# Kernel tuning notes

Hardware: AMD Instinct MI355X
Metric: run time of the kernel (lower is better)

The kernel has to match this reference:

```python
import jax, jax.numpy as jnp
import numpy as np

B, NBLK, D, DY, NDIM, NMC, DH = 4096, 12, 2, 2, 24, 256, 100
SQRT3 = 3.0 ** 0.5
G2 = np.array([[1.0, 0.0], [0.5, SQRT3 / 2.0]], dtype=np.float32)
G = jnp.asarray(np.kron(np.eye(NBLK, dtype=np.float32), G2))  # (24,24) block-diag hexagonal generator
LOG_VOL = (NDIM // 2) * float(np.log(SQRT3 / 2.0))  # log sqrt(det(G G^T))


def _lin(x, w, b=None):
    y = x @ w.T
    return y if b is None else y + b


def _hex_quantize(y):
    # Exact nearest-point quantizer for the product-of-A2 (hexagonal) lattice.
    p = y.reshape(y.shape[:-1] + (NDIM // 2, 2))
    off = jnp.array([0.5, SQRT3 / 2.0], dtype=y.dtype)
    def rnd(q):  # round to rectangular sublattice Z x sqrt(3)Z
        return jnp.stack([jnp.round(q[..., 0]), jnp.round(q[..., 1] / SQRT3) * SQRT3], axis=-1)
    c0 = rnd(p)
    c1 = rnd(p - off) + off
    d0 = jnp.sum((p - c0) ** 2, axis=-1)
    d1 = jnp.sum((p - c1) ** 2, axis=-1)
    return jnp.where((d0 <= d1)[..., None], c0, c1).reshape(y.shape)


def _logits_cumulative(v, Hs, bs, fs):
    # compressai-style per-channel monotone cumulative network. v: (..., C) -> (..., C)
    v = v[..., None]  # (..., C, 1)
    for k in range(len(Hs)):
        v = jnp.einsum('coi,...ci->...co', jax.nn.softplus(Hs[k]), v) + bs[k][:, :, 0]
        if k < len(fs):
            v = v + jnp.tanh(fs[k][:, :, 0]) * jnp.tanh(v)
    return v[..., 0]


def setup_inputs() -> dict:
    key = jax.random.key(0)
    ks = iter(jax.random.split(key, 64))
    def nrm(shape, s=1.0):
        return jax.random.normal(next(ks), shape, jnp.float32) * s
    inp = {}
    inp['x'] = nrm((B, NBLK, D))
    inp['y_mean'] = nrm((NBLK, DY))
    inp['u'] = jax.random.uniform(next(ks), (NMC, NDIM), jnp.float32)
    inp['ga_w0'] = nrm((DH, D), D ** -0.5); inp['ga_b0'] = jnp.zeros((DH,), jnp.float32)
    inp['ga_w1'] = nrm((DH, DH), DH ** -0.5); inp['ga_b1'] = jnp.zeros((DH,), jnp.float32)
    inp['ga_w2'] = nrm((DY, DH), DH ** -0.5); inp['ga_b2'] = jnp.zeros((DY,), jnp.float32)
    inp['gs_w0'] = nrm((DH, DY), DY ** -0.5); inp['gs_b0'] = jnp.zeros((DH,), jnp.float32)
    inp['gs_w1'] = nrm((DH, DH), DH ** -0.5); inp['gs_b1'] = jnp.zeros((DH,), jnp.float32)
    inp['gs_w2'] = nrm((D, DH), DH ** -0.5); inp['gs_b2'] = jnp.zeros((D,), jnp.float32)
    inp['gac_w0'] = nrm((DH, NDIM), NDIM ** -0.5)
    inp['gac_w1'] = nrm((DH, DH), DH ** -0.5)
    inp['gac_w2'] = nrm((NDIM, DH), DH ** -0.5)
    inp['gsc_w0'] = nrm((DH, NDIM), NDIM ** -0.5)
    inp['gsc_w1'] = nrm((DH, DH), DH ** -0.5)
    inp['gsc_w2'] = nrm((NDIM, DH), DH ** -0.5)
    # factorized-prior cumulative params, layer dims 1->3->3->3->3->1
    inp['eb_H0'] = nrm((NDIM, 3, 1), 0.5)
    inp['eb_H1'] = nrm((NDIM, 3, 3), 0.5)
    inp['eb_H2'] = nrm((NDIM, 3, 3), 0.5)
    inp['eb_H3'] = nrm((NDIM, 3, 3), 0.5)
    inp['eb_H4'] = nrm((NDIM, 1, 3), 0.5)
    inp['eb_b0'] = nrm((NDIM, 3, 1), 0.5)
    inp['eb_b1'] = nrm((NDIM, 3, 1), 0.5)
    inp['eb_b2'] = nrm((NDIM, 3, 1), 0.5)
    inp['eb_b3'] = nrm((NDIM, 3, 1), 0.5)
    inp['eb_b4'] = nrm((NDIM, 1, 1), 0.5)
    inp['eb_a0'] = nrm((NDIM, 3, 1), 0.5)
    inp['eb_a1'] = nrm((NDIM, 3, 1), 0.5)
    inp['eb_a2'] = nrm((NDIM, 3, 1), 0.5)
    inp['eb_a3'] = nrm((NDIM, 3, 1), 0.5)
    return inp


def reference(x, y_mean, u, ga_w0, ga_b0, ga_w1, ga_b1, ga_w2, ga_b2,
              gs_w0, gs_b0, gs_w1, gs_b1, gs_w2, gs_b2,
              gac_w0, gac_w1, gac_w2, gsc_w0, gsc_w1, gsc_w2,
              eb_H0, eb_H1, eb_H2, eb_H3, eb_H4,
              eb_b0, eb_b1, eb_b2, eb_b3, eb_b4,
              eb_a0, eb_a1, eb_a2, eb_a3):
    lrelu, sp = jax.nn.leaky_relu, jax.nn.softplus
    # analysis transform g_a: (B, 12, 2) -> (B, 12, dy)
    y1 = _lin(lrelu(_lin(lrelu(_lin(x, ga_w0, ga_b0)), ga_w1, ga_b1)), ga_w2, ga_b2)
    # EMA zero-mean update (buffer assignment => no gradient through the mean)
    ym = jax.lax.stop_gradient(0.05 * y_mean + 0.95 * jnp.mean(y1, axis=0))
    y1 = (y1 - ym).reshape(B, NDIM)
    # coupled analysis transform g_a_c (Softplus MLP, no bias)
    y1 = _lin(sp(_lin(sp(_lin(y1, gac_w0)), gac_w1)), gac_w2)
    # quasi-uniform samples from the Voronoi cell of the lattice origin
    u2 = u @ G
    u2 = u2 - _hex_quantize(u2)
    # lattice quantization with straight-through estimator
    y_q = _hex_quantize(y1)
    y_hat = y1 + jax.lax.stop_gradient(y_q - y1)
    # Monte-Carlo log-likelihood over the Voronoi cell with factorized prior density
    Hs = (eb_H0, eb_H1, eb_H2, eb_H3, eb_H4)
    bs = (eb_b0, eb_b1, eb_b2, eb_b3, eb_b4)
    fs = (eb_a0, eb_a1, eb_a2, eb_a3)
    pts = y_hat[:, None, :] + u2[None, :, :]  # (B, NMC, NDIM)
    def cdf(p):
        return jax.nn.sigmoid(_logits_cumulative(p, Hs, bs, fs))
    _, pdf = jax.jvp(cdf, (pts,), (jnp.ones_like(pts),))  # density = d/dx cdf(x)
    logp = jnp.sum(jnp.log(pdf + 1e-9), axis=-1)  # (B, NMC)
    lik = jax.scipy.special.logsumexp(logp, axis=1) - jnp.log(jnp.float32(NMC)) + LOG_VOL  # (B,)
    # synthesis transforms
    y_hat1 = _lin(sp(_lin(sp(_lin(y_hat, gsc_w0)), gsc_w1)), gsc_w2).reshape(B, NBLK, DY) + ym
    x_hat = _lin(lrelu(_lin(lrelu(_lin(y_hat1, gs_w0, gs_b0)), gs_w1, gs_b1)), gs_w2, gs_b2)
    return (x_hat, lik)
```

## Files before the change

kernel.cpp:

```cpp
#include <hip/hip_runtime.h>
#include <hip/hip_bf16.h>
#include <math.h>

constexpr int NB    = 4096;
constexpr int NBLKc = 12;
constexpr int NDIMc = 24;
constexpr int NMCc  = 256;
constexpr int ROWS2 = NB * NBLKc;

constexpr size_t WS_Y1    = 0;
constexpr size_t WS_YHAT  = 98304;
constexpr size_t WS_YHAT1 = 196608;
constexpr size_t WS_YM    = 294912;
constexpr size_t WS_U2T   = 294936;
constexpr size_t WS_EB    = 301080;
constexpr size_t WS_KMM   = 302472;
constexpr size_t WS_TBL   = 302520;
constexpr size_t WS_END   = WS_TBL + 24 * 64 * 256;

constexpr float STEP_ODD = 0.8660254037844386f;
constexpr float INV_ODD  = 1.1547005383792517f;

__device__ __forceinline__ float lrelu(float x) { return x >= 0.f ? x : 0.01f * x; }

__device__ __forceinline__ float rcp_fast(float x) { return __builtin_amdgcn_rcpf(x); }

__device__ __forceinline__ float tanh_fast(float x) {
    float xx = fminf(fmaxf(x, -15.f), 15.f);
    float e = __expf(xx + xx);
    return fmaf(-2.f, rcp_fast(e + 1.f), 1.f);
}

__device__ __forceinline__ float splus(float x) {
    return fmaxf(x, 0.f) + __logf(1.f + __expf(-fabsf(x)));
}
__device__ __forceinline__ float splus_precise(float x) {
    return fmaxf(x, 0.f) + log1pf(expf(-fabsf(x)));
}

__device__ __forceinline__ void hexq(float p0, float p1, float& q0, float& q1) {
    const float S3 = 1.7320508075688772f;
    const float H3 = 0.8660254037844386f;
    float c00 = rintf(p0);
    float c01 = rintf(p1 / S3) * S3;
    float c10 = rintf(p0 - 0.5f) + 0.5f;
    float c11 = rintf((p1 - H3) / S3) * S3 + H3;
    float d0 = (p0 - c00) * (p0 - c00) + (p1 - c01) * (p1 - c01);
    float d1 = (p0 - c10) * (p0 - c10) + (p1 - c11) * (p1 - c11);
    bool take0 = d0 <= d1;
    q0 = take0 ? c00 : c10;
    q1 = take0 ? c01 : c11;
}

__device__ __forceinline__ float logpdf_ch(const float* __restrict__ P, float p) {
    float w00 = P[0], w01 = P[1], w02 = P[2];
    float z0 = fmaf(w00, p, P[3]);
    float z1 = fmaf(w01, p, P[4]);
    float z2 = fmaf(w02, p, P[5]);
    float a0 = P[6], a1 = P[7], a2 = P[8];
    float e0 = tanh_fast(z0), e1 = tanh_fast(z1), e2 = tanh_fast(z2);
    float h0 = fmaf(a0, e0, z0), h1 = fmaf(a1, e1, z1), h2 = fmaf(a2, e2, z2);
    float t0 = w00 * fmaf(a0, fmaf(-e0, e0, 1.f), 1.f);
    float t1 = w01 * fmaf(a1, fmaf(-e1, e1, 1.f), 1.f);
    float t2 = w02 * fmaf(a2, fmaf(-e2, e2, 1.f), 1.f);

#define EB_LAYER(O)                                                            \
    {                                                                          \
        float z0n = fmaf(P[O+0], h0, fmaf(P[O+1], h1, fmaf(P[O+2], h2, P[O+9])));  \
        float z1n = fmaf(P[O+3], h0, fmaf(P[O+4], h1, fmaf(P[O+5], h2, P[O+10]))); \
        float z2n = fmaf(P[O+6], h0, fmaf(P[O+7], h1, fmaf(P[O+8], h2, P[O+11]))); \
        float s0 = fmaf(P[O+0], t0, fmaf(P[O+1], t1, P[O+2] * t2));            \
        float s1 = fmaf(P[O+3], t0, fmaf(P[O+4], t1, P[O+5] * t2));            \
        float s2 = fmaf(P[O+6], t0, fmaf(P[O+7], t1, P[O+8] * t2));            \
        float g0 = P[O+12], g1 = P[O+13], g2 = P[O+14];                        \
        float q0 = tanh_fast(z0n), q1 = tanh_fast(z1n), q2 = tanh_fast(z2n);   \
        h0 = fmaf(g0, q0, z0n); h1 = fmaf(g1, q1, z1n); h2 = fmaf(g2, q2, z2n); \
        t0 = s0 * fmaf(g0, fmaf(-q0, q0, 1.f), 1.f);                           \
        t1 = s1 * fmaf(g1, fmaf(-q1, q1, 1.f), 1.f);                           \
        t2 = s2 * fmaf(g2, fmaf(-q2, q2, 1.f), 1.f);                           \
    }
    EB_LAYER(9)
    EB_LAYER(24)
    EB_LAYER(39)
#undef EB_LAYER

    float L = fmaf(P[54], h0, fmaf(P[55], h1, fmaf(P[56], h2, P[57])));
    float T = fmaf(P[54], t0, fmaf(P[55], t1, P[56] * t2));
    float Lc = fminf(fmaxf(L, -30.f), 30.f);
    float sg = rcp_fast(1.f + __expf(-Lc));
    float pdf = sg * (1.f - sg) * T;
    return __logf(pdf + 1e-9f);
}

__global__ __launch_bounds__(256) void k_prep(
    const float* __restrict__ H0p, const float* __restrict__ H1p,
    const float* __restrict__ H2p, const float* __restrict__ H3p,
    const float* __restrict__ H4p,
    const float* __restrict__ b0p, const float* __restrict__ b1p,
    const float* __restrict__ b2p, const float* __restrict__ b3p,
    const float* __restrict__ b4p,
    const float* __restrict__ a0p, const float* __restrict__ a1p,
    const float* __restrict__ a2p, const float* __restrict__ a3p,
    const float* __restrict__ u, float* __restrict__ eb, float* __restrict__ u2t)
{
    int tid = threadIdx.x;
    if (tid < 24) {
        int c = tid;
        float* P = eb + c * 58;
        for (int j = 0; j < 3; ++j) P[j]      = splus_precise(H0p[c*3+j]);
        for (int j = 0; j < 3; ++j) P[3+j]    = b0p[c*3+j];
        for (int j = 0; j < 3; ++j) P[6+j]    = tanhf(a0p[c*3+j]);
        for (int j = 0; j < 9; ++j) P[9+j]    = splus_precise(H1p[c*9+j]);
        for (int j = 0; j < 3; ++j) P[18+j]   = b1p[c*3+j];
        for (int j = 0; j < 3; ++j) P[21+j]   = tanhf(a1p[c*3+j]);
        for (int j = 0; j < 9; ++j) P[24+j]   = splus_precise(H2p[c*9+j]);
        for (int j = 0; j < 3; ++j) P[33+j]   = b2p[c*3+j];
        for (int j = 0; j < 3; ++j) P[36+j]   = tanhf(a2p[c*3+j]);
        for (int j = 0; j < 9; ++j) P[39+j]   = splus_precise(H3p[c*9+j]);
        for (int j = 0; j < 3; ++j) P[48+j]   = b3p[c*3+j];
        for (int j = 0; j < 3; ++j) P[51+j]   = tanhf(a3p[c*3+j]);
        for (int j = 0; j < 3; ++j) P[54+j]   = splus_precise(H4p[c*3+j]);
        P[57] = b4p[c];
    }
    int m = tid;
    if (m < 256) {
        for (int j = 0; j < 12; ++j) {
            float a  = u[m*24 + 2*j];
            float bb = u[m*24 + 2*j + 1];
            float p0 = fmaf(0.5f, bb, a);
            float p1 = 0.8660254037844386f * bb;
            float q0, q1; hexq(p0, p1, q0, q1);
            u2t[(2*j)   * 256 + m] = p0 - q0;
            u2t[(2*j+1) * 256 + m] = p1 - q1;
        }
    }
}

__global__ __launch_bounds__(256) void k_mlp2(
    const float* __restrict__ in,
    const float* __restrict__ w0, const float* __restrict__ b0,
    const float* __restrict__ w1, const float* __restrict__ b1,
    const float* __restrict__ w2, const float* __restrict__ b2,
    float* __restrict__ out)
{
    __shared__ alignas(16) float sw1[10000];
    __shared__ alignas(16) float sw0[200];
    __shared__ float sb0[100], sb1[100], sw2[200], sb2[2];
    int tid = threadIdx.x;
    for (int i = tid; i < 10000; i += 256) sw1[i] = w1[i];
    for (int i = tid; i < 200; i += 256) { sw0[i] = w0[i]; sw2[i] = w2[i]; }
    for (int i = tid; i < 100; i += 256) { sb0[i] = b0[i]; sb1[i] = b1[i]; }
    if (tid < 2) sb2[tid] = b2[tid];
    __syncthreads();

    int r = tid >> 2, q = tid & 3;
    int row = blockIdx.x * 64 + r;
    float x0 = in[2*row], x1 = in[2*row + 1];

    float h[100];
#pragma unroll
    for (int j = 0; j < 100; ++j)
        h[j] = lrelu(fmaf(sw0[2*j], x0, fmaf(sw0[2*j+1], x1, sb0[j])));

    float y0 = 0.f, y1 = 0.f;
    int i0 = q * 25;
    for (int i = i0; i < i0 + 25; ++i) {
        const float4* wr = (const float4*)&sw1[i * 100];
        float s = sb1[i];
#pragma unroll
        for (int jj = 0; jj < 25; ++jj) {
            float4 w = wr[jj];
            s = fmaf(w.x, h[4*jj], s);
            s = fmaf(w.y, h[4*jj+1], s);
            s = fmaf(w.z, h[4*jj+2], s);
            s = fmaf(w.w, h[4*jj+3], s);
        }
        float a = lrelu(s);
        y0 = fmaf(sw2[i], a, y0);
        y1 = fmaf(sw2[100 + i], a, y1);
    }
    y0 += __shfl_xor(y0, 1); y0 += __shfl_xor(y0, 2);
    y1 += __shfl_xor(y1, 1); y1 += __shfl_xor(y1, 2);
    if (q == 0) {
        out[2*row]     = y0 + sb2[0];
        out[2*row + 1] = y1 + sb2[1];
    }
}

__global__ __launch_bounds__(256) void k_mean(
    const float* __restrict__ y1, const float* __restrict__ y_mean,
    float* __restrict__ ym)
{
    __shared__ float red[96];
    int tid = threadIdx.x;
    float acc[24];
#pragma unroll
    for (int c = 0; c < 24; ++c) acc[c] = 0.f;
    for (int b = tid; b < NB; b += 256) {
        const float4* rp = (const float4*)&y1[b * 24];
#pragma unroll
        for (int k = 0; k < 6; ++k) {
            float4 v = rp[k];
            acc[4*k]   += v.x; acc[4*k+1] += v.y;
            acc[4*k+2] += v.z; acc[4*k+3] += v.w;
        }
    }
#pragma unroll
    for (int c = 0; c < 24; ++c) {
        float v = acc[c];
        for (int off = 1; off < 64; off <<= 1) v += __shfl_xor(v, off);
        if ((tid & 63) == 0) red[(tid >> 6) * 24 + c] = v;
    }
    __syncthreads();
    if (tid < 24) {
        float sv = red[tid] + red[24 + tid] + red[48 + tid] + red[72 + tid];
        ym[tid] = fmaf(0.05f, y_mean[tid], 0.95f * (sv * (1.0f / NB)));
    }
}

template <int MODE>
__global__ __launch_bounds__(256) void k_mlp24(
    const float* __restrict__ in,
    const float* __restrict__ w0, const float* __restrict__ w1,
    const float* __restrict__ w2,
    const float* __restrict__ ymg, float* __restrict__ out)
{
    __shared__ alignas(16) float sw0[2400];
    __shared__ alignas(16) float sw1[10000];
    __shared__ alignas(16) float sw2[2400];
    __shared__ alignas(16) float X[16 * 24];
    __shared__ alignas(16) float Ha[16 * 100];
    __shared__ alignas(16) float Hb[16 * 100];
    __shared__ float O[16 * 24];
    __shared__ float sym[24];

    int tid = threadIdx.x;
    int row0 = blockIdx.x * 16;
    for (int i = tid; i < 2400; i += 256) { sw0[i] = w0[i]; sw2[i] = w2[i]; }
    for (int i = tid; i < 10000; i += 256) sw1[i] = w1[i];
    if (tid < 24) sym[tid] = ymg[tid];
    for (int e = tid; e < 16 * 24; e += 256) {
        float v = in[row0 * 24 + e];
        if (MODE == 0) v -= ymg[e % 24];
        X[e] = v;
    }
    __syncthreads();

    int r = tid >> 4, s = tid & 15;
    for (int k = 0; k < 7; ++k) {
        int i = s + 16 * k;
        if (i < 100) {
            const float4* wr = (const float4*)&sw0[i * 24];
            const float4* xr = (const float4*)&X[r * 24];
            float acc = 0.f;
#pragma unroll
            for (int jj = 0; jj < 6; ++jj) {
                float4 w = wr[jj], xv = xr[jj];
                acc = fmaf(w.x, xv.x, acc); acc = fmaf(w.y, xv.y, acc);
                acc = fmaf(w.z, xv.z, acc); acc = fmaf(w.w, xv.w, acc);
            }
            Ha[r * 100 + i] = splus(acc);
        }
    }
    __syncthreads();
    for (int k = 0; k < 7; ++k) {
        int i = s + 16 * k;
        if (i < 100) {
            const float4* wr = (const float4*)&sw1[i * 100];
            const float4* hr = (const float4*)&Ha[r * 100];
            float acc = 0.f;
#pragma unroll
            for (int jj = 0; jj < 25; ++jj) {
                float4 w = wr[jj], hv = hr[jj];
                acc = fmaf(w.x, hv.x, acc); acc = fmaf(w.y, hv.y, acc);
                acc = fmaf(w.z, hv.z, acc); acc = fmaf(w.w, hv.w, acc);
            }
            Hb[r * 100 + i] = splus(acc);
        }
    }
    __syncthreads();
    for (int e = tid; e < 16 * 24; e += 256) {
        int rr = e / 24, c = e - rr * 24;
        const float4* wr = (const float4*)&sw2[c * 100];
        const float4* hr = (const float4*)&Hb[rr * 100];
        float acc = 0.f;
#pragma unroll
        for (int jj = 0; jj < 25; ++jj) {
            float4 w = wr[jj], hv = hr[jj];
            acc = fmaf(w.x, hv.x, acc); acc = fmaf(w.y, hv.y, acc);
            acc = fmaf(w.z, hv.z, acc); acc = fmaf(w.w, hv.w, acc);
        }
        O[rr * 24 + c] = acc;
    }
    __syncthreads();
    if (MODE == 0) {
        for (int e = tid; e < 16 * 12; e += 256) {
            int rr = e / 12, pr = e - rr * 12;
            float p0 = O[rr * 24 + 2*pr], p1 = O[rr * 24 + 2*pr + 1];
            float q0, q1; hexq(p0, p1, q0, q1);
            out[(row0 + rr) * 24 + 2*pr]     = q0;
            out[(row0 + rr) * 24 + 2*pr + 1] = q1;
        }
    } else {
        for (int e = tid; e < 16 * 24; e += 256) {
            int rr = e / 24, c = e - rr * 24;
            out[(row0 + rr) * 24 + c] = O[rr * 24 + c] + sym[c];
        }
    }
}

__global__ __launch_bounds__(256) void k_minmax(
    const float* __restrict__ yhat, int* __restrict__ kmm)
{
    __shared__ int smin[4], smax[4];
    int c = blockIdx.x;
    float inv = (c & 1) ? INV_ODD : 2.0f;
    int tid = threadIdx.x;
    int kmin = 0x7fffffff, kmax = 0x80000000;
    for (int b = tid; b < NB; b += 256) {
        int k = (int)rintf(yhat[b * 24 + c] * inv);
        kmin = min(kmin, k);
        kmax = max(kmax, k);
    }
    for (int off = 1; off < 64; off <<= 1) {
        kmin = min(kmin, __shfl_xor(kmin, off));
        kmax = max(kmax, __shfl_xor(kmax, off));
    }
    if ((tid & 63) == 0) { smin[tid >> 6] = kmin; smax[tid >> 6] = kmax; }
    __syncthreads();
    if (tid == 0) {
        kmm[c]      = min(min(smin[0], smin[1]), min(smin[2], smin[3]));
        kmm[24 + c] = max(max(smax[0], smax[1]), max(smax[2], smax[3]));
    }
}

__global__ __launch_bounds__(256) void k_table(
    const float* __restrict__ eb, const float* __restrict__ u2t,
    const int* __restrict__ kmm, float* __restrict__ tbl)
{
    int cv = blockIdx.x;
    int c = cv >> 6, v = cv & 63;
    int m = threadIdx.x;
    float step = (c & 1) ? STEP_ODD : 0.5f;
    float val = (float)(kmm[c] + v) * step;
    float p = val + u2t[c * 256 + m];
    tbl[cv * 256 + m] = logpdf_ch(eb + c * 58, p);
}

__global__ __launch_bounds__(256) void k_mc_tbl(
    const float* __restrict__ yhat, const float* __restrict__ u2t,
    const float* __restrict__ eb, const int* __restrict__ kmm,
    const float* __restrict__ tbl, float* __restrict__ lik)
{
    __shared__ float red[256];
    int tid = threadIdx.x;
    int b = blockIdx.x;

    float y[24];
    const float4* yr = (const float4*)(yhat + b * 24);
#pragma unroll
    for (int k4 = 0; k4 < 6; ++k4) {
        float4 t = yr[k4];
        y[4*k4] = t.x; y[4*k4+1] = t.y; y[4*k4+2] = t.z; y[4*k4+3] = t.w;
    }

    float lp = 0.f;
    unsigned miss = 0;
#pragma unroll
    for (int c = 0; c < 24; ++c) {
        float inv = (c & 1) ? INV_ODD : 2.0f;
        int k = (int)rintf(y[c] * inv);
        int idx = k - kmm[c];
        if (idx >= 0 && idx < 64)
            lp += tbl[(c * 64 + idx) * 256 + tid];
        else
            miss |= (1u << c);
    }
    while (miss) {
        int c = __ffs(miss) - 1;
        miss &= miss - 1;
        lp += logpdf_ch(eb + c * 58, y[c] + u2t[c * 256 + tid]);
    }

    red[tid] = lp;
    __syncthreads();
    for (int s = 128; s > 0; s >>= 1) {
        if (tid < s) red[tid] = fmaxf(red[tid], red[tid + s]);
        __syncthreads();
    }
    float mx = red[0];
    __syncthreads();
    red[tid] = __expf(lp - mx);
    __syncthreads();
    for (int s = 128; s > 0; s >>= 1) {
        if (tid < s) red[tid] += red[tid + s];
        __syncthreads();
    }
    if (tid == 0)
        lik[b] = mx + __logf(red[0]) - 7.271269879190247f;
}

__global__ __launch_bounds__(256) void k_mc_direct(
    const float* __restrict__ yhat, const float* __restrict__ u2t,
    const float* __restrict__ eb, float* __restrict__ lik)
{
    __shared__ alignas(16) float sU[24 * 256];
    __shared__ float red[256];
    int tid = threadIdx.x;
    int b = blockIdx.x;
    for (int i = tid; i < 1536; i += 256)
        ((float4*)sU)[i] = ((const float4*)u2t)[i];
    __syncthreads();

    float lp = 0.f;
    for (int c = 0; c < 24; ++c) {
        float p = yhat[b * 24 + c] + sU[c * 256 + tid];
        lp += logpdf_ch(eb + c * 58, p);
    }

    red[tid] = lp;
    __syncthreads();
    for (int s = 128; s > 0; s >>= 1) {
        if (tid < s) red[tid] = fmaxf(red[tid], red[tid + s]);
        __syncthreads();
    }
    float mx = red[0];
    __syncthreads();
    red[tid] = __expf(lp - mx);
    __syncthreads();
    for (int s = 128; s > 0; s >>= 1) {
        if (tid < s) red[tid] += red[tid + s];
        __syncthreads();
    }
    if (tid == 0)
        lik[b] = mx + __logf(red[0]) - 7.271269879190247f;
}

extern "C" void kernel_launch(void* const* d_in, const int* in_sizes, int n_in,
                              void* d_out, int out_size, void* d_ws, size_t ws_size,
                              hipStream_t stream)
{
    (void)in_sizes; (void)n_in; (void)out_size;
    const float* x      = (const float*)d_in[0];
    const float* y_mean = (const float*)d_in[1];
    const float* u      = (const float*)d_in[2];
    const float* ga_w0  = (const float*)d_in[3];
    const float* ga_b0  = (const float*)d_in[4];
    const float* ga_w1  = (const float*)d_in[5];
    const float* ga_b1  = (const float*)d_in[6];
    const float* ga_w2  = (const float*)d_in[7];
    const float* ga_b2  = (const float*)d_in[8];
    const float* gs_w0  = (const float*)d_in[9];
    const float* gs_b0  = (const float*)d_in[10];
    const float* gs_w1  = (const float*)d_in[11];
    const float* gs_b1  = (const float*)d_in[12];
    const float* gs_w2  = (const float*)d_in[13];
    const float* gs_b2  = (const float*)d_in[14];
    const float* gac_w0 = (const float*)d_in[15];
    const float* gac_w1 = (const float*)d_in[16];
    const float* gac_w2 = (const float*)d_in[17];
    const float* gsc_w0 = (const float*)d_in[18];
    const float* gsc_w1 = (const float*)d_in[19];
    const float* gsc_w2 = (const float*)d_in[20];
    const float* eb_H0  = (const float*)d_in[21];
    const float* eb_H1  = (const float*)d_in[22];
    const float* eb_H2  = (const float*)d_in[23];
    const float* eb_H3  = (const float*)d_in[24];
    const float* eb_H4  = (const float*)d_in[25];
    const float* eb_b0  = (const float*)d_in[26];
    const float* eb_b1  = (const float*)d_in[27];
    const float* eb_b2  = (const float*)d_in[28];
    const float* eb_b3  = (const float*)d_in[29];
    const float* eb_b4  = (const float*)d_in[30];
    const float* eb_a0  = (const float*)d_in[31];
    const float* eb_a1  = (const float*)d_in[32];
    const float* eb_a2  = (const float*)d_in[33];
    const float* eb_a3  = (const float*)d_in[34];

    float* ws    = (float*)d_ws;
    float* y1    = ws + WS_Y1;
    float* yhat  = ws + WS_YHAT;
    float* yhat1 = ws + WS_YHAT1;
    float* ym    = ws + WS_YM;
    float* u2t   = ws + WS_U2T;
    float* eb    = ws + WS_EB;
    int*   kmm   = (int*)(ws + WS_KMM);
    float* tbl   = ws + WS_TBL;
    float* xhat  = (float*)d_out;
    float* lik   = (float*)d_out + 98304;

    bool use_tbl = ws_size >= WS_END * sizeof(float);

    k_prep<<<1, 256, 0, stream>>>(eb_H0, eb_H1, eb_H2, eb_H3, eb_H4,
                                  eb_b0, eb_b1, eb_b2, eb_b3, eb_b4,
                                  eb_a0, eb_a1, eb_a2, eb_a3, u, eb, u2t);
    k_mlp2<<<ROWS2 / 64, 256, 0, stream>>>(x, ga_w0, ga_b0, ga_w1, ga_b1,
                                           ga_w2, ga_b2, y1);
    k_mean<<<1, 256, 0, stream>>>(y1, y_mean, ym);
    k_mlp24<0><<<NB / 16, 256, 0, stream>>>(y1, gac_w0, gac_w1, gac_w2, ym, yhat);
    if (use_tbl) {
        k_minmax<<<24, 256, 0, stream>>>(yhat, kmm);
        k_table<<<24 * 64, 256, 0, stream>>>(eb, u2t, kmm, tbl);
    }
    k_mlp24<1><<<NB / 16, 256, 0, stream>>>(yhat, gsc_w0, gsc_w1, gsc_w2, ym, yhat1);
    k_mlp2<<<ROWS2 / 64, 256, 0, stream>>>(yhat1, gs_w0, gs_b0, gs_w1, gs_b1,
                                           gs_w2, gs_b2, xhat);
    if (use_tbl)
        k_mc_tbl<<<NB, 256, 0, stream>>>(yhat, u2t, eb, kmm, tbl, lik);
    else
        k_mc_direct<<<NB, 256, 0, stream>>>(yhat, u2t, eb, lik);
}
```

Baseline: 129.5 us.

## Fuse mean and minmax reductions into MLP kernels and restructure MLP work split

Several changes land together. The y1 mean is folded into the first 2-wide MLP as per-block partial sums, and the quantized-index min/max goes into the mlp24 quantize stage through shared and global atomics. This drops the separate k_mean and k_minmax kernels. k_mlp2 now gives each thread a full row, with no 4-way split or shuffle reduction, and runs on 4x fewer blocks. k_mlp24 moves to 64 rows per 512-thread block with register-held inputs and an 8-way split over hidden units, and the softmax reductions use wave shuffles instead of a shared-memory tree. The risks are that 192 blocks of k_mlp2 may underfill the GPU, and that register pressure rises from the h[100] and acc[24] arrays.

```diff
diff --git a/kernel.cpp b/kernel.cpp
--- a/kernel.cpp
+++ b/kernel.cpp
@@ -1,12 +1,12 @@
 #include <hip/hip_runtime.h>
 #include <hip/hip_bf16.h>
 #include <math.h>
+#include <limits.h>
 
 constexpr int NB    = 4096;
 constexpr int NBLKc = 12;
-constexpr int NDIMc = 24;
-constexpr int NMCc  = 256;
 constexpr int ROWS2 = NB * NBLKc;
+constexpr int MLP2_BLOCKS = ROWS2 / 256;
 
 constexpr size_t WS_Y1    = 0;
 constexpr size_t WS_YHAT  = 98304;
@@ -15,14 +15,14 @@
 constexpr size_t WS_U2T   = 294936;
 constexpr size_t WS_EB    = 301080;
 constexpr size_t WS_KMM   = 302472;
-constexpr size_t WS_TBL   = 302520;
+constexpr size_t WS_PART  = 302520;
+constexpr size_t WS_TBL   = 307128;
 constexpr size_t WS_END   = WS_TBL + 24 * 64 * 256;
 
 constexpr float STEP_ODD = 0.8660254037844386f;
 constexpr float INV_ODD  = 1.1547005383792517f;
 
 __device__ __forceinline__ float lrelu(float x) { return x >= 0.f ? x : 0.01f * x; }
-
 __device__ __forceinline__ float rcp_fast(float x) { return __builtin_amdgcn_rcpf(x); }
 
 __device__ __forceinline__ float tanh_fast(float x) {
@@ -30,7 +30,6 @@
     float e = __expf(xx + xx);
     return fmaf(-2.f, rcp_fast(e + 1.f), 1.f);
 }
-
 __device__ __forceinline__ float splus(float x) {
     return fmaxf(x, 0.f) + __logf(1.f + __expf(-fabsf(x)));
 }
@@ -101,7 +100,8 @@
     const float* __restrict__ b4p,
     const float* __restrict__ a0p, const float* __restrict__ a1p,
     const float* __restrict__ a2p, const float* __restrict__ a3p,
-    const float* __restrict__ u, float* __restrict__ eb, float* __restrict__ u2t)
+    const float* __restrict__ u, float* __restrict__ eb, float* __restrict__ u2t,
+    int* __restrict__ kmm)
 {
     int tid = threadIdx.x;
     if (tid < 24) {
@@ -121,6 +121,8 @@
         for (int j = 0; j < 3; ++j) P[51+j]   = tanhf(a3p[c*3+j]);
         for (int j = 0; j < 3; ++j) P[54+j]   = splus_precise(H4p[c*3+j]);
         P[57] = b4p[c];
+        kmm[tid]      = INT_MAX;
+        kmm[24 + tid] = INT_MIN;
     }
     int m = tid;
     if (m < 256) {
@@ -136,16 +138,17 @@
     }
 }
 
+template <int MEAN>
 __global__ __launch_bounds__(256) void k_mlp2(
     const float* __restrict__ in,
     const float* __restrict__ w0, const float* __restrict__ b0,
     const float* __restrict__ w1, const float* __restrict__ b1,
     const float* __restrict__ w2, const float* __restrict__ b2,
-    float* __restrict__ out)
+    float* __restrict__ out, float* __restrict__ partial)
 {
     __shared__ alignas(16) float sw1[10000];
-    __shared__ alignas(16) float sw0[200];
-    __shared__ float sb0[100], sb1[100], sw2[200], sb2[2];
+    __shared__ float sw0[200], sb0[100], sb1[100], sw2[200], sb2[2];
+    __shared__ float S[256][2];
     int tid = threadIdx.x;
     for (int i = tid; i < 10000; i += 256) sw1[i] = w1[i];
     for (int i = tid; i < 200; i += 256) { sw0[i] = w0[i]; sw2[i] = w2[i]; }
@@ -153,18 +156,18 @@
     if (tid < 2) sb2[tid] = b2[tid];
     __syncthreads();
 
-    int r = tid >> 2, q = tid & 3;
-    int row = blockIdx.x * 64 + r;
-    float x0 = in[2*row], x1 = in[2*row + 1];
+    int row = blockIdx.x * 256 + tid;
+    float2 xv = ((const float2*)in)[row];
+    float x0 = xv.x, x1 = xv.y;
 
     float h[100];
 #pragma unroll
     for (int j = 0; j < 100; ++j)
         h[j] = lrelu(fmaf(sw0[2*j], x0, fmaf(sw0[2*j+1], x1, sb0[j])));
 
-    float y0 = 0.f, y1 = 0.f;
-    int i0 = q * 25;
-    for (int i = i0; i < i0 + 25; ++i) {
+    float y0 = sb2[0], y1 = sb2[1];
+#pragma unroll 2
+    for (int i = 0; i < 100; ++i) {
         const float4* wr = (const float4*)&sw1[i * 100];
         float s = sb1[i];
 #pragma unroll
@@ -179,158 +182,155 @@
         y0 = fmaf(sw2[i], a, y0);
         y1 = fmaf(sw2[100 + i], a, y1);
     }
-    y0 += __shfl_xor(y0, 1); y0 += __shfl_xor(y0, 2);
-    y1 += __shfl_xor(y1, 1); y1 += __shfl_xor(y1, 2);
-    if (q == 0) {
-        out[2*row]     = y0 + sb2[0];
-        out[2*row + 1] = y1 + sb2[1];
-    }
-}
-
-__global__ __launch_bounds__(256) void k_mean(
-    const float* __restrict__ y1, const float* __restrict__ y_mean,
+    float2 yv; yv.x = y0; yv.y = y1;
+    ((float2*)out)[row] = yv;
+
+    if (MEAN) {
+        S[tid][0] = y0; S[tid][1] = y1;
+        __syncthreads();
+        if (tid < 24) {
+            int j = tid >> 1, par = tid & 1;
+            int row0 = blockIdx.x * 256;
+            int k0 = ((j - row0) % 12 + 12) % 12;
+            float s = 0.f;
+            for (int k = k0; k < 256; k += 12) s += S[k][par];
+            partial[blockIdx.x * 24 + tid] = s;
+        }
+    }
+}
+
+__global__ __launch_bounds__(256) void k_mean_final(
+    const float* __restrict__ partial, const float* __restrict__ y_mean,
     float* __restrict__ ym)
 {
-    __shared__ float red[96];
     int tid = threadIdx.x;
-    float acc[24];
-#pragma unroll
-    for (int c = 0; c < 24; ++c) acc[c] = 0.f;
-    for (int b = tid; b < NB; b += 256) {
-        const float4* rp = (const float4*)&y1[b * 24];
-#pragma unroll
-        for (int k = 0; k < 6; ++k) {
-            float4 v = rp[k];
-            acc[4*k]   += v.x; acc[4*k+1] += v.y;
-            acc[4*k+2] += v.z; acc[4*k+3] += v.w;
-        }
-    }
-#pragma unroll
-    for (int c = 0; c < 24; ++c) {
-        float v = acc[c];
-        for (int off = 1; off < 64; off <<= 1) v += __shfl_xor(v, off);
-        if ((tid & 63) == 0) red[(tid >> 6) * 24 + c] = v;
-    }
-    __syncthreads();
-    if (tid < 24) {
-        float sv = red[tid] + red[24 + tid] + red[48 + tid] + red[72 + tid];
-        ym[tid] = fmaf(0.05f, y_mean[tid], 0.95f * (sv * (1.0f / NB)));
-    }
+    int c = tid >> 3, s = tid & 7;
+    float v = 0.f;
+    if (c < 24)
+        for (int g = s; g < MLP2_BLOCKS; g += 8) v += partial[g * 24 + c];
+    v += __shfl_xor(v, 1); v += __shfl_xor(v, 2); v += __shfl_xor(v, 4);
+    if (c < 24 && s == 0)
+        ym[c] = fmaf(0.05f, y_mean[c], 0.95f * (v * (1.0f / NB)));
 }
 
 template <int MODE>
-__global__ __launch_bounds__(256) void k_mlp24(
+__global__ __launch_bounds__(512) void k_mlp24(
     const float* __restrict__ in,
     const float* __restrict__ w0, const float* __restrict__ w1,
     const float* __restrict__ w2,
-    const float* __restrict__ ymg, float* __restrict__ out)
+    const float* __restrict__ ymg, float* __restrict__ out,
+    int* __restrict__ kmm)
 {
     __shared__ alignas(16) float sw0[2400];
     __shared__ alignas(16) float sw1[10000];
     __shared__ alignas(16) float sw2[2400];
-    __shared__ alignas(16) float X[16 * 24];
-    __shared__ alignas(16) float Ha[16 * 100];
-    __shared__ alignas(16) float Hb[16 * 100];
-    __shared__ float O[16 * 24];
-    __shared__ float sym[24];
+    __shared__ float h0L[64 * 101];
+    __shared__ float P[8 * 64 * 25];
+    __shared__ float symL[24];
+    __shared__ int kminL[24], kmaxL[24];
 
     int tid = threadIdx.x;
-    int row0 = blockIdx.x * 16;
-    for (int i = tid; i < 2400; i += 256) { sw0[i] = w0[i]; sw2[i] = w2[i]; }
-    for (int i = tid; i < 10000; i += 256) sw1[i] = w1[i];
-    if (tid < 24) sym[tid] = ymg[tid];
-    for (int e = tid; e < 16 * 24; e += 256) {
-        float v = in[row0 * 24 + e];
-        if (MODE == 0) v -= ymg[e % 24];
-        X[e] = v;
-    }
-    __syncthreads();
-
-    int r = tid >> 4, s = tid & 15;
-    for (int k = 0; k < 7; ++k) {
-        int i = s + 16 * k;
-        if (i < 100) {
-            const float4* wr = (const float4*)&sw0[i * 24];
-            const float4* xr = (const float4*)&X[r * 24];
-            float acc = 0.f;
-#pragma unroll
-            for (int jj = 0; jj < 6; ++jj) {
-                float4 w = wr[jj], xv = xr[jj];
-                acc = fmaf(w.x, xv.x, acc); acc = fmaf(w.y, xv.y, acc);
-                acc = fmaf(w.z, xv.z, acc); acc = fmaf(w.w, xv.w, acc);
+    int q = tid >> 6, lane = tid & 63;
+    int row0 = blockIdx.x * 64;
+    int row = row0 + lane;
+
+    for (int i = tid; i < 2400; i += 512) { sw0[i] = w0[i]; sw2[i] = w2[i]; }
+    for (int i = tid; i < 10000; i += 512) sw1[i] = w1[i];
+    if (tid < 24) {
+        symL[tid] = ymg[tid];
+        kminL[tid] = INT_MAX; kmaxL[tid] = INT_MIN;
+    }
+
+    float xr[24];
+    const float4* xp = (const float4*)(in + row * 24);
+#pragma unroll
+    for (int k = 0; k < 6; ++k) {
+        float4 t = xp[k];
+        xr[4*k] = t.x; xr[4*k+1] = t.y; xr[4*k+2] = t.z; xr[4*k+3] = t.w;
+    }
+    __syncthreads();
+    if (MODE == 0) {
+#pragma unroll
+        for (int j = 0; j < 24; ++j) xr[j] -= symL[j];
+    }
+
+    int i0 = q * 12 + min(q, 4);
+    int cnt = (q < 4) ? 13 : 12;
+
+    for (int ii = 0; ii < cnt; ++ii) {
+        int i = i0 + ii;
+        const float4* wr = (const float4*)&sw0[i * 24];
+        float acc = 0.f;
+#pragma unroll
+        for (int jj = 0; jj < 6; ++jj) {
+            float4 w = wr[jj];
+            acc = fmaf(w.x, xr[4*jj], acc);
+            acc = fmaf(w.y, xr[4*jj+1], acc);
+            acc = fmaf(w.z, xr[4*jj+2], acc);
+            acc = fmaf(w.w, xr[4*jj+3], acc);
+        }
+        h0L[lane * 101 + i] = splus(acc);
+    }
+    __syncthreads();
+
+    float h[100];
+#pragma unroll
+    for (int j = 0; j < 100; ++j) h[j] = h0L[lane * 101 + j];
+
+    float acc[24];
+#pragma unroll
+    for (int c = 0; c < 24; ++c) acc[c] = 0.f;
+    for (int ii = 0; ii < cnt; ++ii) {
+        int i = i0 + ii;
+        const float4* wr = (const float4*)&sw1[i * 100];
+        float s = 0.f;
+#pragma unroll
+        for (int jj = 0; jj < 25; ++jj) {
+            float4 w = wr[jj];
+            s = fmaf(w.x, h[4*jj], s);
+            s = fmaf(w.y, h[4*jj+1], s);
+            s = fmaf(w.z, h[4*jj+2], s);
+            s = fmaf(w.w, h[4*jj+3], s);
+        }
+        float a = splus(s);
+#pragma unroll
+        for (int c = 0; c < 24; ++c)
+            acc[c] = fmaf(sw2[c * 100 + i], a, acc[c]);
+    }
+#pragma unroll
+    for (int c = 0; c < 24; ++c) P[(q * 64 + lane) * 25 + c] = acc[c];
+    __syncthreads();
+
+    if (MODE == 0) {
+        for (int e = tid; e < 64 * 12; e += 512) {
+            int r = e / 12, pr = e - r * 12;
+            float v0 = 0.f, v1 = 0.f;
+#pragma unroll
+            for (int qq = 0; qq < 8; ++qq) {
+                v0 += P[(qq * 64 + r) * 25 + 2*pr];
+                v1 += P[(qq * 64 + r) * 25 + 2*pr + 1];
             }
-            Ha[r * 100 + i] = splus(acc);
-        }
-    }
-    __syncthreads();
-    for (int k = 0; k < 7; ++k) {
-        int i = s + 16 * k;
-        if (i < 100) {
-            const float4* wr = (const float4*)&sw1[i * 100];
-            const float4* hr = (const float4*)&Ha[r * 100];
-            float acc = 0.f;
-#pragma unroll
-            for (int jj = 0; jj < 25; ++jj) {
-                float4 w = wr[jj], hv = hr[jj];
-                acc = fmaf(w.x, hv.x, acc); acc = fmaf(w.y, hv.y, acc);
-                acc = fmaf(w.z, hv.z, acc); acc = fmaf(w.w, hv.w, acc);
-            }
-            Hb[r * 100 + i] = splus(acc);
-        }
-    }
-    __syncthreads();
-    for (int e = tid; e < 16 * 24; e += 256) {
-        int rr = e / 24, c = e - rr * 24;
-        const float4* wr = (const float4*)&sw2[c * 100];
-        const float4* hr = (const float4*)&Hb[rr * 100];
-        float acc = 0.f;
-#pragma unroll
-        for (int jj = 0; jj < 25; ++jj) {
-            float4 w = wr[jj], hv = hr[jj];
-            acc = fmaf(w.x, hv.x, acc); acc = fmaf(w.y, hv.y, acc);
-            acc = fmaf(w.z, hv.z, acc); acc = fmaf(w.w, hv.w, acc);
-        }
-        O[rr * 24 + c] = acc;
-    }
-    __syncthreads();
-    if (MODE == 0) {
-        for (int e = tid; e < 16 * 12; e += 256) {
-            int rr = e / 12, pr = e - rr * 12;
-            float p0 = O[rr * 24 + 2*pr], p1 = O[rr * 24 + 2*pr + 1];
-            float q0, q1; hexq(p0, p1, q0, q1);
-            out[(row0 + rr) * 24 + 2*pr]     = q0;
-            out[(row0 + rr) * 24 + 2*pr + 1] = q1;
+            float q0, q1; hexq(v0, v1, q0, q1);
+            out[(row0 + r) * 24 + 2*pr]     = q0;
+            out[(row0 + r) * 24 + 2*pr + 1] = q1;
+            int k0 = (int)rintf(q0 * 2.0f);
+            int k1 = (int)rintf(q1 * INV_ODD);
+            atomicMin(&kminL[2*pr], k0);     atomicMax(&kmaxL[2*pr], k0);
+            atomicMin(&kminL[2*pr + 1], k1); atomicMax(&kmaxL[2*pr + 1], k1);
+        }
+        __syncthreads();
+        if (tid < 24) {
+            atomicMin(&kmm[tid], kminL[tid]);
+            atomicMax(&kmm[24 + tid], kmaxL[tid]);
         }
     } else {
-        for (int e = tid; e < 16 * 24; e += 256) {
-            int rr = e / 24, c = e - rr * 24;
-            out[(row0 + rr) * 24 + c] = O[rr * 24 + c] + sym[c];
-        }
-    }
-}
-
-__global__ __launch_bounds__(256) void k_minmax(
-    const float* __restrict__ yhat, int* __restrict__ kmm)
-{
-    __shared__ int smin[4], smax[4];
-    int c = blockIdx.x;
-    float inv = (c & 1) ? INV_ODD : 2.0f;
-    int tid = threadIdx.x;
-    int kmin = 0x7fffffff, kmax = 0x80000000;
-    for (int b = tid; b < NB; b += 256) {
-        int k = (int)rintf(yhat[b * 24 + c] * inv);
-        kmin = min(kmin, k);
-        kmax = max(kmax, k);
-    }
-    for (int off = 1; off < 64; off <<= 1) {
-        kmin = min(kmin, __shfl_xor(kmin, off));
-        kmax = max(kmax, __shfl_xor(kmax, off));
-    }
-    if ((tid & 63) == 0) { smin[tid >> 6] = kmin; smax[tid >> 6] = kmax; }
-    __syncthreads();
-    if (tid == 0) {
-        kmm[c]      = min(min(smin[0], smin[1]), min(smin[2], smin[3]));
-        kmm[24 + c] = max(max(smax[0], smax[1]), max(smax[2], smax[3]));
+        for (int e = tid; e < 64 * 24; e += 512) {
+            int r = e / 24, c = e - r * 24;
+            float v = 0.f;
+#pragma unroll
+            for (int qq = 0; qq < 8; ++qq) v += P[(qq * 64 + r) * 25 + c];
+            out[(row0 + r) * 24 + c] = v + symL[c];
+        }
     }
 }
 
@@ -352,8 +352,9 @@
     const float* __restrict__ eb, const int* __restrict__ kmm,
     const float* __restrict__ tbl, float* __restrict__ lik)
 {
-    __shared__ float red[256];
+    __shared__ float redm[4], reds[4];
     int tid = threadIdx.x;
+    int wv = tid >> 6;
     int b = blockIdx.x;
 
     float y[24];
@@ -382,22 +383,20 @@
         lp += logpdf_ch(eb + c * 58, y[c] + u2t[c * 256 + tid]);
     }
 
-    red[tid] = lp;
-    __syncthreads();
-    for (int s = 128; s > 0; s >>= 1) {
-        if (tid < s) red[tid] = fmaxf(red[tid], red[tid + s]);
-        __syncthreads();
-    }
-    float mx = red[0];
-    __syncthreads();
-    red[tid] = __expf(lp - mx);
-    __syncthreads();
-    for (int s = 128; s > 0; s >>= 1) {
-        if (tid < s) red[tid] += red[tid + s];
-        __syncthreads();
-    }
+    float m = lp;
+#pragma unroll
+    for (int off = 1; off < 64; off <<= 1) m = fmaxf(m, __shfl_xor(m, off));
+    if ((tid & 63) == 0) redm[wv] = m;
+    __syncthreads();
+    float mx = fmaxf(fmaxf(redm[0], redm[1]), fmaxf(redm[2], redm[3]));
+    float e = __expf(lp - mx);
+#pragma unroll
+    for (int off = 1; off < 64; off <<= 1) e += __shfl_xor(e, off);
+    if ((tid & 63) == 0) reds[wv] = e;
+    __syncthreads();
     if (tid == 0)
-        lik[b] = mx + __logf(red[0]) - 7.271269879190247f;
+        lik[b] = mx + __logf(reds[0] + reds[1] + reds[2] + reds[3])
+               - 7.271269879190247f;
 }
 
 __global__ __launch_bounds__(256) void k_mc_direct(
@@ -405,35 +404,32 @@
     const float* __restrict__ eb, float* __restrict__ lik)
 {
     __shared__ alignas(16) float sU[24 * 256];
-    __shared__ float red[256];
+    __shared__ float redm[4], reds[4];
     int tid = threadIdx.x;
+    int wv = tid >> 6;
     int b = blockIdx.x;
     for (int i = tid; i < 1536; i += 256)
         ((float4*)sU)[i] = ((const float4*)u2t)[i];
     __syncthreads();
 
     float lp = 0.f;
-    for (int c = 0; c < 24; ++c) {
-        float p = yhat[b * 24 + c] + sU[c * 256 + tid];
-        lp += logpdf_ch(eb + c * 58, p);
-    }
-
-    red[tid] = lp;
-    __syncthreads();
-    for (int s = 128; s > 0; s >>= 1) {
-        if (tid < s) red[tid] = fmaxf(red[tid], red[tid + s]);
-        __syncthreads();
-    }
-    float mx = red[0];
-    __syncthreads();
-    red[tid] = __expf(lp - mx);
-    __syncthreads();
-    for (int s = 128; s > 0; s >>= 1) {
-        if (tid < s) red[tid] += red[tid + s];
-        __syncthreads();
-    }
+    for (int c = 0; c < 24; ++c)
+        lp += logpdf_ch(eb + c * 58, yhat[b * 24 + c] + sU[c * 256 + tid]);
+
+    float m = lp;
+#pragma unroll
+    for (int off = 1; off < 64; off <<= 1) m = fmaxf(m, __shfl_xor(m, off));
+    if ((tid & 63) == 0) redm[wv] = m;
+    __syncthreads();
+    float mx = fmaxf(fmaxf(redm[0], redm[1]), fmaxf(redm[2], redm[3]));
+    float e = __expf(lp - mx);
+#pragma unroll
+    for (int off = 1; off < 64; off <<= 1) e += __shfl_xor(e, off);
+    if ((tid & 63) == 0) reds[wv] = e;
+    __syncthreads();
     if (tid == 0)
-        lik[b] = mx + __logf(red[0]) - 7.271269879190247f;
+        lik[b] = mx + __logf(reds[0] + reds[1] + reds[2] + reds[3])
+               - 7.271269879190247f;
 }
 
 extern "C" void kernel_launch(void* const* d_in, const int* in_sizes, int n_in,
@@ -485,6 +481,7 @@
     float* u2t   = ws + WS_U2T;
     float* eb    = ws + WS_EB;
     int*   kmm   = (int*)(ws + WS_KMM);
+    float* part  = ws + WS_PART;
     float* tbl   = ws + WS_TBL;
     float* xhat  = (float*)d_out;
     float* lik   = (float*)d_out + 98304;
@@ -493,18 +490,18 @@
 
     k_prep<<<1, 256, 0, stream>>>(eb_H0, eb_H1, eb_H2, eb_H3, eb_H4,
                                   eb_b0, eb_b1, eb_b2, eb_b3, eb_b4,
-                                  eb_a0, eb_a1, eb_a2, eb_a3, u, eb, u2t);
-    k_mlp2<<<ROWS2 / 64, 256, 0, stream>>>(x, ga_w0, ga_b0, ga_w1, ga_b1,
-                                           ga_w2, ga_b2, y1);
-    k_mean<<<1, 256, 0, stream>>>(y1, y_mean, ym);
-    k_mlp24<0><<<NB / 16, 256, 0, stream>>>(y1, gac_w0, gac_w1, gac_w2, ym, yhat);
-    if (use_tbl) {
-        k_minmax<<<24, 256, 0, stream>>>(yhat, kmm);
+                                  eb_a0, eb_a1, eb_a2, eb_a3, u, eb, u2t, kmm);
+    k_mlp2<1><<<MLP2_BLOCKS, 256, 0, stream>>>(x, ga_w0, ga_b0, ga_w1, ga_b1,
+                                               ga_w2, ga_b2, y1, part);
+    k_mean_final<<<1, 256, 0, stream>>>(part, y_mean, ym);
+    k_mlp24<0><<<NB / 64, 512, 0, stream>>>(y1, gac_w0, gac_w1, gac_w2, ym,
+                                            yhat, kmm);
+    if (use_tbl)
         k_table<<<24 * 64, 256, 0, stream>>>(eb, u2t, kmm, tbl);
-    }
-    k_mlp24<1><<<NB / 16, 256, 0, stream>>>(yhat, gsc_w0, gsc_w1, gsc_w2, ym, yhat1);
-    k_mlp2<<<ROWS2 / 64, 256, 0, stream>>>(yhat1, gs_w0, gs_b0, gs_w1, gs_b1,
-                                           gs_w2, gs_b2, xhat);
+    k_mlp24<1><<<NB / 64, 512, 0, stream>>>(yhat, gsc_w0, gsc_w1, gsc_w2, ym,
+                                            yhat1, kmm);
+    k_mlp2<0><<<MLP2_BLOCKS, 256, 0, stream>>>(yhat1, gs_w0, gs_b0, gs_w1, gs_b1,
+                                               gs_w2, gs_b2, xhat, nullptr);
     if (use_tbl)
         k_mc_tbl<<<NB, 256, 0, stream>>>(yhat, u2t, eb, kmm, tbl, lik);
     else
```

Measured after the change: 171.9 us. +32.8%, slower.
